# Kernel optimization log

Hardware: AMD Instinct MI355X
Metric: run time of the kernel (lower is better)

The kernel has to match this reference:

```python
import jax, jax.numpy as jnp
import numpy as np

H, HS, E, T, B, PF = 16, 64, 1024, 2048, 4, 4

def setup_inputs() -> dict:
    key = jax.random.key(0)
    ks = jax.random.split(key, 12)
    s = 0.02
    return {
        "x":  jax.random.normal(ks[0], (B, T, E), jnp.float32),
        "Wq": jax.random.normal(ks[1], (H, E, HS), jnp.float32) * s,
        "Wk": jax.random.normal(ks[2], (H, E, HS), jnp.float32) * s,
        "Wv": jax.random.normal(ks[3], (H, E, HS), jnp.float32) * s,
        "Wp": jax.random.normal(ks[4], (E, E), jnp.float32) * s,
        "bp": jnp.zeros((E,), jnp.float32),
        "W1": jax.random.normal(ks[5], (E, PF * E), jnp.float32) * s,
        "b1": jnp.zeros((PF * E,), jnp.float32),
        "W2": jax.random.normal(ks[6], (PF * E, E), jnp.float32) * s,
        "b2": jnp.zeros((E,), jnp.float32),
        "g1": jnp.ones((E,), jnp.float32),
        "be1": jnp.zeros((E,), jnp.float32),
        "g2": jnp.ones((E,), jnp.float32),
        "be2": jnp.zeros((E,), jnp.float32),
    }

def _layernorm(x, gain, bias, eps=1e-5):
    # torch.var default is unbiased (ddof=1) -- faithful to the source
    mean = jnp.mean(x, axis=-1, keepdims=True)
    var = jnp.sum((x - mean) ** 2, axis=-1, keepdims=True) / (x.shape[-1] - 1)
    return (x - mean) / jnp.sqrt(var + eps) * gain + bias

def reference(x, Wq, Wk, Wv, Wp, bp, W1, b1, W2, b2, g1, be1, g2, be2):
    Bv, Tv, Ev = x.shape
    hs = Wq.shape[-1]
    h = _layernorm(x, g1, be1)
    # all heads at once: [B,T,E] x [H,E,hs] -> [B,H,T,hs]
    q = jnp.einsum("bte,hed->bhtd", h, Wq)
    k = jnp.einsum("bte,hed->bhtd", h, Wk)
    v = jnp.einsum("bte,hed->bhtd", h, Wv)
    # NOTE: source multiplies by 1/hs**(-0.5) == sqrt(hs); kept faithful
    scores = jnp.einsum("bhtd,bhsd->bhts", q, k) * (hs ** 0.5)
    causal = jnp.tril(jnp.ones((Tv, Tv), bool))
    scores = jnp.where(causal, scores, -jnp.inf)
    w = jax.nn.softmax(scores, axis=-1)
    o = jnp.einsum("bhts,bhsd->bhtd", w, v)
    # concat heads (head 0 first) -> [B,T,H*hs]
    o = o.transpose(0, 2, 1, 3).reshape(Bv, Tv, -1)
    o = o @ Wp + bp
    x = x + o
    h2 = _layernorm(x, g2, be2)
    ff = jax.nn.relu(h2 @ W1 + b1) @ W2 + b2
    return x + ff
```

## Files before the change

### kernel.cpp

```cpp
#include <hip/hip_runtime.h>
#include <hip/hip_bf16.h>
#include <cstdint>

typedef __bf16 bf16_t;
typedef bf16_t bf16x8 __attribute__((ext_vector_type(8)));
typedef float f32x4 __attribute__((ext_vector_type(4)));

#define DEVI __device__ __forceinline__

DEVI void gload_lds16(const void* g, void* l) {
    __builtin_amdgcn_global_load_lds((const __attribute__((address_space(1))) void*)g,
                                     (__attribute__((address_space(3))) void*)l, 16, 0, 0);
}

__global__ __launch_bounds__(256) void transpose_f32_bf16(
    const float* __restrict__ src, bf16_t* __restrict__ dst,
    int ldsrc, int lddst, long srcBatchStride, long dstBatchStride)
{
    __shared__ float tile[32][33];
    src += (long)blockIdx.z * srcBatchStride;
    dst += (long)blockIdx.z * dstBatchStride;
    const int bx = blockIdx.x * 32;
    const int by = blockIdx.y * 32;
    const int tx = threadIdx.x, ty = threadIdx.y;
    #pragma unroll
    for (int j = 0; j < 32; j += 8)
        tile[ty + j][tx] = src[(size_t)(by + ty + j) * ldsrc + bx + tx];
    __syncthreads();
    #pragma unroll
    for (int j = 0; j < 32; j += 8)
        dst[(size_t)(bx + ty + j) * lddst + by + tx] = (bf16_t)tile[tx][ty + j];
}

__global__ __launch_bounds__(256) void ln_kernel(
    const float* __restrict__ x, const float* __restrict__ g,
    const float* __restrict__ b, bf16_t* __restrict__ out)
{
    const int row = blockIdx.x;
    const int tid = threadIdx.x;
    __shared__ float red[8];
    const float4 v = ((const float4*)(x + (size_t)row * 1024))[tid];
    float s = v.x + v.y + v.z + v.w;
    #pragma unroll
    for (int m = 32; m; m >>= 1) s += __shfl_xor(s, m);
    if ((tid & 63) == 0) red[tid >> 6] = s;
    __syncthreads();
    const float mean = (red[0] + red[1] + red[2] + red[3]) * (1.f / 1024.f);
    const float dx = v.x - mean, dy = v.y - mean, dz = v.z - mean, dw = v.w - mean;
    float ss = dx * dx + dy * dy + dz * dz + dw * dw;
    #pragma unroll
    for (int m = 32; m; m >>= 1) ss += __shfl_xor(ss, m);
    if ((tid & 63) == 0) red[4 + (tid >> 6)] = ss;
    __syncthreads();
    const float var = (red[4] + red[5] + red[6] + red[7]) * (1.f / 1023.f);
    const float rstd = rsqrtf(var + 1e-5f);
    const float4 gv = ((const float4*)g)[tid];
    const float4 bv = ((const float4*)b)[tid];
    union { bf16_t h[4]; uint2 u; } pk;
    pk.h[0] = (bf16_t)(dx * rstd * gv.x + bv.x);
    pk.h[1] = (bf16_t)(dy * rstd * gv.y + bv.y);
    pk.h[2] = (bf16_t)(dz * rstd * gv.z + bv.z);
    pk.h[3] = (bf16_t)(dw * rstd * gv.w + bv.w);
    *((uint2*)(out + (size_t)row * 1024 + tid * 4)) = pk.u;
}

template <int EPI>
__global__ __launch_bounds__(256) void gemm_bt(
    const bf16_t* __restrict__ A, const bf16_t* __restrict__ BT,
    void* __restrict__ Cout, const float* __restrict__ bias,
    const float* __restrict__ res, int M, int N, int K)
{
    constexpr int BK = 64;
    __shared__ bf16_t As[128 * BK];
    __shared__ bf16_t Bs[128 * BK];
    const int tid = threadIdx.x;
    const int lane = tid & 63;
    const int wid = tid >> 6;
    const int m0 = blockIdx.y * 128, n0 = blockIdx.x * 128;
    const int lrow = lane & 15, lgrp = lane >> 4;
    const int mw = (wid >> 1) * 64, nw = (wid & 1) * 64;
    f32x4 acc[4][4] = {};

    for (int k0 = 0; k0 < K; k0 += BK) {
        __syncthreads();
        #pragma unroll
        for (int i = 0; i < 4; ++i) {
            const int c = i * 256 + tid;
            const int row = c >> 3, kc = (c & 7) * 8;
            gload_lds16(A + (size_t)(m0 + row) * K + k0 + kc, &As[c * 8]);
        }
        #pragma unroll
        for (int i = 0; i < 4; ++i) {
            const int c = i * 256 + tid;
            const int row = c >> 3, kc = (c & 7) * 8;
            gload_lds16(BT + (size_t)(n0 + row) * K + k0 + kc, &Bs[c * 8]);
        }
        __syncthreads();
        #pragma unroll
        for (int kk = 0; kk < BK; kk += 32) {
            bf16x8 af[4], bfr[4];
            #pragma unroll
            for (int mi = 0; mi < 4; ++mi)
                af[mi] = *(const bf16x8*)&As[(mw + mi * 16 + lrow) * BK + kk + lgrp * 8];
            #pragma unroll
            for (int ni = 0; ni < 4; ++ni)
                bfr[ni] = *(const bf16x8*)&Bs[(nw + ni * 16 + lrow) * BK + kk + lgrp * 8];
            #pragma unroll
            for (int mi = 0; mi < 4; ++mi)
                #pragma unroll
                for (int ni = 0; ni < 4; ++ni)
                    acc[mi][ni] = __builtin_amdgcn_mfma_f32_16x16x32_bf16(
                        af[mi], bfr[ni], acc[mi][ni], 0, 0, 0);
        }
    }

    #pragma unroll
    for (int mi = 0; mi < 4; ++mi) {
        #pragma unroll
        for (int r = 0; r < 4; ++r) {
            const int row = m0 + mw + mi * 16 + lgrp * 4 + r;
            #pragma unroll
            for (int ni = 0; ni < 4; ++ni) {
                const int col = n0 + nw + ni * 16 + lrow;
                const float v = acc[mi][ni][r];
                if (EPI == 0) {
                    ((bf16_t*)Cout)[(size_t)row * N + col] = (bf16_t)v;
                } else if (EPI == 1) {
                    ((float*)Cout)[(size_t)row * N + col] =
                        v + bias[col] + res[(size_t)row * N + col];
                } else {
                    const float t = v + bias[col];
                    ((bf16_t*)Cout)[(size_t)row * N + col] = (bf16_t)(t > 0.f ? t : 0.f);
                }
            }
        }
    }
}

__global__ __launch_bounds__(256) void attn_kernel(
    const bf16_t* __restrict__ qkv, bf16_t* __restrict__ O)
{
    const int tid = threadIdx.x, lane = tid & 63, wid = tid >> 6;
    const int lrow = lane & 15, lgrp = lane >> 4;
    const int qb = (15 - blockIdx.x) * 128;
    const int b = blockIdx.y >> 4, h = blockIdx.y & 15;
    const bf16_t* base  = qkv + (size_t)b * 2048 * 3072;
    const bf16_t* Kbase = base + 1024 + h * 64;
    const bf16_t* Vbase = base + 2048 + h * 64;

    __shared__ bf16_t Vt[64 * 64];
    __shared__ bf16_t Pl[4][32 * 64];

    const int mw = wid * 32;

    bf16x8 qf[2][2];
    #pragma unroll
    for (int mi = 0; mi < 2; ++mi)
        #pragma unroll
        for (int dh = 0; dh < 2; ++dh) {
            bf16x8 t = *(const bf16x8*)(base + (size_t)(qb + mw + mi * 16 + lrow) * 3072
                                        + h * 64 + dh * 32 + lgrp * 8);
            #pragma unroll
            for (int j = 0; j < 8; ++j) t[j] = (bf16_t)((float)t[j] * 8.0f);
            qf[mi][dh] = t;
        }

    f32x4 of[2][4] = {};
    float m_r[2][4], l_r[2][4];
    #pragma unroll
    for (int mi = 0; mi < 2; ++mi)
        #pragma unroll
        for (int r = 0; r < 4; ++r) { m_r[mi][r] = -INFINITY; l_r[mi][r] = 0.f; }

    const int kvlen = qb + 128;
    for (int kv = 0; kv < kvlen; kv += 64) {
        __syncthreads();
        #pragma unroll
        for (int i = 0; i < 2; ++i) {
            const int key = tid & 63;
            const int dc8 = (tid >> 6) + i * 4;
            const bf16x8 vv = *(const bf16x8*)(Vbase + (size_t)(kv + key) * 3072 + dc8 * 8);
            #pragma unroll
            for (int j = 0; j < 8; ++j)
                Vt[(dc8 * 8 + j) * 64 + (((key >> 3) ^ j) << 3) + (key & 7)] = vv[j];
        }
        __syncthreads();

        const bool act0 = (kv <= qb + mw + 15);
        const bool act1 = (kv <= qb + mw + 31);
        if (act1) {
            bf16x8 kf[4][2];
            #pragma unroll
            for (int kt = 0; kt < 4; ++kt)
                #pragma unroll
                for (int dh = 0; dh < 2; ++dh)
                    kf[kt][dh] = *(const bf16x8*)(Kbase + (size_t)(kv + kt * 16 + lrow) * 3072
                                                  + dh * 32 + lgrp * 8);

            #pragma unroll
            for (int mi = 0; mi < 2; ++mi) {
                if (mi == 0 && !act0) continue;
                f32x4 s[4] = {};
                #pragma unroll
                for (int kt = 0; kt < 4; ++kt) {
                    s[kt] = __builtin_amdgcn_mfma_f32_16x16x32_bf16(qf[mi][0], kf[kt][0], s[kt], 0, 0, 0);
                    s[kt] = __builtin_amdgcn_mfma_f32_16x16x32_bf16(qf[mi][1], kf[kt][1], s[kt], 0, 0, 0);
                }
                float p[4][4];
                #pragma unroll
                for (int r = 0; r < 4; ++r) {
                    const int q = qb + mw + mi * 16 + lgrp * 4 + r;
                    float v0 = (kv + 0 * 16 + lrow <= q) ? s[0][r] : -INFINITY;
                    float v1 = (kv + 1 * 16 + lrow <= q) ? s[1][r] : -INFINITY;
                    float v2 = (kv + 2 * 16 + lrow <= q) ? s[2][r] : -INFINITY;
                    float v3 = (kv + 3 * 16 + lrow <= q) ? s[3][r] : -INFINITY;
                    float mx = fmaxf(fmaxf(v0, v1), fmaxf(v2, v3));
                    #pragma unroll
                    for (int mm = 8; mm; mm >>= 1) mx = fmaxf(mx, __shfl_xor(mx, mm));
                    const float mnew = fmaxf(m_r[mi][r], mx);
                    const float alpha = __expf(m_r[mi][r] - mnew);
                    p[0][r] = __expf(v0 - mnew);
                    p[1][r] = __expf(v1 - mnew);
                    p[2][r] = __expf(v2 - mnew);
                    p[3][r] = __expf(v3 - mnew);
                    float rs = p[0][r] + p[1][r] + p[2][r] + p[3][r];
                    #pragma unroll
                    for (int mm = 8; mm; mm >>= 1) rs += __shfl_xor(rs, mm);
                    l_r[mi][r] = l_r[mi][r] * alpha + rs;
                    m_r[mi][r] = mnew;
                    #pragma unroll
                    for (int dg = 0; dg < 4; ++dg) of[mi][dg][r] *= alpha;
                }
                #pragma unroll
                for (int kt = 0; kt < 4; ++kt)
                    #pragma unroll
                    for (int r = 0; r < 4; ++r) {
                        const int qi = mi * 16 + lgrp * 4 + r;
                        const int ki = kt * 16 + lrow;
                        Pl[wid][qi * 64 + ((((ki >> 3) ^ (qi & 7))) << 3) + (ki & 7)] = (bf16_t)p[kt][r];
                    }
            }
            asm volatile("s_waitcnt lgkmcnt(0)" ::: "memory");
            __builtin_amdgcn_sched_barrier(0);

            bf16x8 vf[4][2];
            #pragma unroll
            for (int dg = 0; dg < 4; ++dg) {
                const int d = dg * 16 + lrow;
                #pragma unroll
                for (int kh = 0; kh < 2; ++kh)
                    vf[dg][kh] = *(const bf16x8*)&Vt[d * 64 + ((((kh * 4 + lgrp) ^ (d & 7))) << 3)];
            }
            #pragma unroll
            for (int mi = 0; mi < 2; ++mi) {
                if (mi == 0 && !act0) continue;
                const int qrow = mi * 16 + lrow;
                #pragma unroll
                for (int kh = 0; kh < 2; ++kh) {
                    const bf16x8 pf = *(const bf16x8*)&Pl[wid][qrow * 64 + ((((kh * 4 + lgrp) ^ (lrow & 7))) << 3)];
                    #pragma unroll
                    for (int dg = 0; dg < 4; ++dg)
                        of[mi][dg] = __builtin_amdgcn_mfma_f32_16x16x32_bf16(pf, vf[dg][kh], of[mi][dg], 0, 0, 0);
                }
            }
        }
    }

    #pragma unroll
    for (int mi = 0; mi < 2; ++mi)
        #pragma unroll
        for (int dg = 0; dg < 4; ++dg)
            #pragma unroll
            for (int r = 0; r < 4; ++r) {
                const size_t row = (size_t)b * 2048 + qb + mw + mi * 16 + lgrp * 4 + r;
                O[row * 1024 + h * 64 + dg * 16 + lrow] = (bf16_t)(of[mi][dg][r] / l_r[mi][r]);
            }
}

extern "C" void kernel_launch(void* const* d_in, const int* in_sizes, int n_in,
                              void* d_out, int out_size, void* d_ws, size_t ws_size,
                              hipStream_t stream)
{
    const float* x   = (const float*)d_in[0];
    const float* Wq  = (const float*)d_in[1];
    const float* Wk  = (const float*)d_in[2];
    const float* Wv  = (const float*)d_in[3];
    const float* Wp  = (const float*)d_in[4];
    const float* bp  = (const float*)d_in[5];
    const float* W1  = (const float*)d_in[6];
    const float* b1  = (const float*)d_in[7];
    const float* W2  = (const float*)d_in[8];
    const float* b2  = (const float*)d_in[9];
    const float* g1  = (const float*)d_in[10];
    const float* be1 = (const float*)d_in[11];
    const float* g2  = (const float*)d_in[12];
    const float* be2 = (const float*)d_in[13];

    char* w = (char*)d_ws;
    auto alloc = [&](size_t bytes) { char* p = w; w += (bytes + 255) & ~255ull; return p; };
    bf16_t* wqkvT = (bf16_t*)alloc((size_t)3072 * 1024 * 2);
    bf16_t* wpT   = (bf16_t*)alloc((size_t)1024 * 1024 * 2);
    bf16_t* w1T   = (bf16_t*)alloc((size_t)4096 * 1024 * 2);
    bf16_t* w2T   = (bf16_t*)alloc((size_t)1024 * 4096 * 2);
    bf16_t* h     = (bf16_t*)alloc((size_t)8192 * 1024 * 2);
    bf16_t* qkv   = (bf16_t*)alloc((size_t)8192 * 3072 * 2);
    float*  x2    = (float*)alloc((size_t)8192 * 1024 * 4);
    bf16_t* act   = (bf16_t*)alloc((size_t)8192 * 4096 * 2);
    bf16_t* o     = h;
    bf16_t* h2    = qkv;

    const dim3 tblk(32, 8);
    transpose_f32_bf16<<<dim3(2, 32, 16), tblk, 0, stream>>>(Wq, wqkvT,                64, 1024, 1024 * 64, 64 * 1024);
    transpose_f32_bf16<<<dim3(2, 32, 16), tblk, 0, stream>>>(Wk, wqkvT + 1024 * 1024,  64, 1024, 1024 * 64, 64 * 1024);
    transpose_f32_bf16<<<dim3(2, 32, 16), tblk, 0, stream>>>(Wv, wqkvT + 2048 * 1024,  64, 1024, 1024 * 64, 64 * 1024);
    transpose_f32_bf16<<<dim3(32, 32, 1),  tblk, 0, stream>>>(Wp, wpT, 1024, 1024, 0, 0);
    transpose_f32_bf16<<<dim3(128, 32, 1), tblk, 0, stream>>>(W1, w1T, 4096, 1024, 0, 0);
    transpose_f32_bf16<<<dim3(32, 128, 1), tblk, 0, stream>>>(W2, w2T, 1024, 4096, 0, 0);

    ln_kernel<<<8192, 256, 0, stream>>>(x, g1, be1, h);
    gemm_bt<0><<<dim3(24, 64), 256, 0, stream>>>(h, wqkvT, qkv, nullptr, nullptr, 8192, 3072, 1024);
    attn_kernel<<<dim3(16, 64), 256, 0, stream>>>(qkv, o);
    gemm_bt<1><<<dim3(8, 64), 256, 0, stream>>>(o, wpT, x2, bp, x, 8192, 1024, 1024);
    ln_kernel<<<8192, 256, 0, stream>>>(x2, g2, be2, h2);
    gemm_bt<2><<<dim3(32, 64), 256, 0, stream>>>(h2, w1T, act, b1, nullptr, 8192, 4096, 1024);
    gemm_bt<1><<<dim3(8, 64), 256, 0, stream>>>(act, w2T, d_out, b2, x2, 8192, 1024, 4096);
}
```

Before: 769.4 us.

## Pair causal query blocks per CTA and prefetch next K/V tile into registers

Each attention block now handles two query tiles (jq and 15-jq), so every CTA does the same amount of causal work and the grid shrinks to 8x64. K and V for the next 64-key tile are loaded into registers while the current tile is computed, hiding global load latency. The row-sum shuffle reduction moves out of the inner loop to a single reduction at the end, and s_setprio wraps the MFMA sections. The cost is higher register pressure from the prefetch buffers and fewer, longer blocks, which may lower occupancy.

```diff
diff --git a/kernel.cpp b/kernel.cpp
--- a/kernel.cpp
+++ b/kernel.cpp
@@ -142,7 +142,6 @@
 {
     const int tid = threadIdx.x, lane = tid & 63, wid = tid >> 6;
     const int lrow = lane & 15, lgrp = lane >> 4;
-    const int qb = (15 - blockIdx.x) * 128;
     const int b = blockIdx.y >> 4, h = blockIdx.y & 15;
     const bf16_t* base  = qkv + (size_t)b * 2048 * 3072;
     const bf16_t* Kbase = base + 1024 + h * 64;
@@ -152,129 +151,172 @@
     __shared__ bf16_t Pl[4][32 * 64];
 
     const int mw = wid * 32;
-
-    bf16x8 qf[2][2];
-    #pragma unroll
-    for (int mi = 0; mi < 2; ++mi)
-        #pragma unroll
-        for (int dh = 0; dh < 2; ++dh) {
-            bf16x8 t = *(const bf16x8*)(base + (size_t)(qb + mw + mi * 16 + lrow) * 3072
-                                        + h * 64 + dh * 32 + lgrp * 8);
-            #pragma unroll
-            for (int j = 0; j < 8; ++j) t[j] = (bf16_t)((float)t[j] * 8.0f);
-            qf[mi][dh] = t;
-        }
-
-    f32x4 of[2][4] = {};
-    float m_r[2][4], l_r[2][4];
-    #pragma unroll
-    for (int mi = 0; mi < 2; ++mi)
-        #pragma unroll
-        for (int r = 0; r < 4; ++r) { m_r[mi][r] = -INFINITY; l_r[mi][r] = 0.f; }
-
-    const int kvlen = qb + 128;
-    for (int kv = 0; kv < kvlen; kv += 64) {
-        __syncthreads();
-        #pragma unroll
-        for (int i = 0; i < 2; ++i) {
-            const int key = tid & 63;
-            const int dc8 = (tid >> 6) + i * 4;
-            const bf16x8 vv = *(const bf16x8*)(Vbase + (size_t)(kv + key) * 3072 + dc8 * 8);
-            #pragma unroll
-            for (int j = 0; j < 8; ++j)
-                Vt[(dc8 * 8 + j) * 64 + (((key >> 3) ^ j) << 3) + (key & 7)] = vv[j];
-        }
-        __syncthreads();
-
-        const bool act0 = (kv <= qb + mw + 15);
-        const bool act1 = (kv <= qb + mw + 31);
-        if (act1) {
-            bf16x8 kf[4][2];
-            #pragma unroll
-            for (int kt = 0; kt < 4; ++kt)
-                #pragma unroll
-                for (int dh = 0; dh < 2; ++dh)
-                    kf[kt][dh] = *(const bf16x8*)(Kbase + (size_t)(kv + kt * 16 + lrow) * 3072
-                                                  + dh * 32 + lgrp * 8);
-
-            #pragma unroll
-            for (int mi = 0; mi < 2; ++mi) {
-                if (mi == 0 && !act0) continue;
-                f32x4 s[4] = {};
-                #pragma unroll
-                for (int kt = 0; kt < 4; ++kt) {
-                    s[kt] = __builtin_amdgcn_mfma_f32_16x16x32_bf16(qf[mi][0], kf[kt][0], s[kt], 0, 0, 0);
-                    s[kt] = __builtin_amdgcn_mfma_f32_16x16x32_bf16(qf[mi][1], kf[kt][1], s[kt], 0, 0, 0);
-                }
-                float p[4][4];
+    const int vkey = tid & 63;
+    const int vdc  = tid >> 6;
+
+    for (int pass = 0; pass < 2; ++pass) {
+        const int jq = (pass == 0) ? 15 - (int)blockIdx.x : (int)blockIdx.x;
+        const int qb = jq * 128;
+        const int nt = (qb + 128) >> 6;
+
+        bf16x8 qf[2][2];
+        #pragma unroll
+        for (int mi = 0; mi < 2; ++mi)
+            #pragma unroll
+            for (int dh = 0; dh < 2; ++dh) {
+                bf16x8 t = *(const bf16x8*)(base + (size_t)(qb + mw + mi * 16 + lrow) * 3072
+                                            + h * 64 + dh * 32 + lgrp * 8);
+                #pragma unroll
+                for (int j = 0; j < 8; ++j) t[j] = (bf16_t)((float)t[j] * 8.0f);
+                qf[mi][dh] = t;
+            }
+
+        f32x4 of[2][4] = {};
+        float m_r[2][4], l_r[2][4];
+        #pragma unroll
+        for (int mi = 0; mi < 2; ++mi)
+            #pragma unroll
+            for (int r = 0; r < 4; ++r) { m_r[mi][r] = -INFINITY; l_r[mi][r] = 0.f; }
+
+        bf16x8 vvc[2], kfc[4][2];
+        #pragma unroll
+        for (int i = 0; i < 2; ++i)
+            vvc[i] = *(const bf16x8*)(Vbase + (size_t)vkey * 3072 + (vdc + i * 4) * 8);
+        #pragma unroll
+        for (int kt = 0; kt < 4; ++kt)
+            #pragma unroll
+            for (int dh = 0; dh < 2; ++dh)
+                kfc[kt][dh] = *(const bf16x8*)(Kbase + (size_t)(kt * 16 + lrow) * 3072
+                                               + dh * 32 + lgrp * 8);
+
+        for (int t = 0; t < nt; ++t) {
+            const int kv = t << 6;
+            __syncthreads();
+            #pragma unroll
+            for (int i = 0; i < 2; ++i) {
+                const int dc8 = vdc + i * 4;
+                #pragma unroll
+                for (int j = 0; j < 8; ++j)
+                    Vt[(dc8 * 8 + j) * 64 + (((vkey >> 3) ^ j) << 3) + (vkey & 7)] = vvc[i][j];
+            }
+            __syncthreads();
+
+            bf16x8 vvn[2], kfn[4][2];
+            const bool hasn = (t + 1 < nt);
+            if (hasn) {
+                const int kv2 = kv + 64;
+                #pragma unroll
+                for (int i = 0; i < 2; ++i)
+                    vvn[i] = *(const bf16x8*)(Vbase + (size_t)(kv2 + vkey) * 3072 + (vdc + i * 4) * 8);
+                #pragma unroll
+                for (int kt = 0; kt < 4; ++kt)
+                    #pragma unroll
+                    for (int dh = 0; dh < 2; ++dh)
+                        kfn[kt][dh] = *(const bf16x8*)(Kbase + (size_t)(kv2 + kt * 16 + lrow) * 3072
+                                                       + dh * 32 + lgrp * 8);
+            }
+
+            const bool act0 = (kv <= qb + mw + 15);
+            const bool act1 = (kv <= qb + mw + 31);
+            if (act1) {
+                #pragma unroll
+                for (int mi = 0; mi < 2; ++mi) {
+                    if (mi == 0 && !act0) continue;
+                    f32x4 s[4] = {};
+                    __builtin_amdgcn_s_setprio(1);
+                    #pragma unroll
+                    for (int kt = 0; kt < 4; ++kt) {
+                        s[kt] = __builtin_amdgcn_mfma_f32_16x16x32_bf16(qf[mi][0], kfc[kt][0], s[kt], 0, 0, 0);
+                        s[kt] = __builtin_amdgcn_mfma_f32_16x16x32_bf16(qf[mi][1], kfc[kt][1], s[kt], 0, 0, 0);
+                    }
+                    __builtin_amdgcn_s_setprio(0);
+                    float p[4][4];
+                    #pragma unroll
+                    for (int r = 0; r < 4; ++r) {
+                        const int q = qb + mw + mi * 16 + lgrp * 4 + r;
+                        float v0 = (kv + 0 * 16 + lrow <= q) ? s[0][r] : -INFINITY;
+                        float v1 = (kv + 1 * 16 + lrow <= q) ? s[1][r] : -INFINITY;
+                        float v2 = (kv + 2 * 16 + lrow <= q) ? s[2][r] : -INFINITY;
+                        float v3 = (kv + 3 * 16 + lrow <= q) ? s[3][r] : -INFINITY;
+                        float mx = fmaxf(fmaxf(v0, v1), fmaxf(v2, v3));
+                        #pragma unroll
+                        for (int mm = 8; mm; mm >>= 1) mx = fmaxf(mx, __shfl_xor(mx, mm));
+                        const float mnew = fmaxf(m_r[mi][r], mx);
+                        const float alpha = __expf(m_r[mi][r] - mnew);
+                        p[0][r] = __expf(v0 - mnew);
+                        p[1][r] = __expf(v1 - mnew);
+                        p[2][r] = __expf(v2 - mnew);
+                        p[3][r] = __expf(v3 - mnew);
+                        l_r[mi][r] = l_r[mi][r] * alpha + (p[0][r] + p[1][r] + p[2][r] + p[3][r]);
+                        m_r[mi][r] = mnew;
+                        #pragma unroll
+                        for (int dg = 0; dg < 4; ++dg) of[mi][dg][r] *= alpha;
+                    }
+                    #pragma unroll
+                    for (int kt = 0; kt < 4; ++kt)
+                        #pragma unroll
+                        for (int r = 0; r < 4; ++r) {
+                            const int qi = mi * 16 + lgrp * 4 + r;
+                            const int ki = kt * 16 + lrow;
+                            Pl[wid][qi * 64 + ((((ki >> 3) ^ (qi & 7))) << 3) + (ki & 7)] = (bf16_t)p[kt][r];
+                        }
+                }
+                asm volatile("s_waitcnt lgkmcnt(0)" ::: "memory");
+                __builtin_amdgcn_sched_barrier(0);
+
+                bf16x8 vf[4][2];
+                #pragma unroll
+                for (int dg = 0; dg < 4; ++dg) {
+                    const int d = dg * 16 + lrow;
+                    #pragma unroll
+                    for (int kh = 0; kh < 2; ++kh)
+                        vf[dg][kh] = *(const bf16x8*)&Vt[d * 64 + ((((kh * 4 + lgrp) ^ (d & 7))) << 3)];
+                }
+                __builtin_amdgcn_s_setprio(1);
+                #pragma unroll
+                for (int mi = 0; mi < 2; ++mi) {
+                    if (mi == 0 && !act0) continue;
+                    const int qrow = mi * 16 + lrow;
+                    #pragma unroll
+                    for (int kh = 0; kh < 2; ++kh) {
+                        const bf16x8 pf = *(const bf16x8*)&Pl[wid][qrow * 64 + ((((kh * 4 + lgrp) ^ (lrow & 7))) << 3)];
+                        #pragma unroll
+                        for (int dg = 0; dg < 4; ++dg)
+                            of[mi][dg] = __builtin_amdgcn_mfma_f32_16x16x32_bf16(pf, vf[dg][kh], of[mi][dg], 0, 0, 0);
+                    }
+                }
+                __builtin_amdgcn_s_setprio(0);
+            }
+
+            if (hasn) {
+                #pragma unroll
+                for (int i = 0; i < 2; ++i) vvc[i] = vvn[i];
+                #pragma unroll
+                for (int kt = 0; kt < 4; ++kt)
+                    #pragma unroll
+                    for (int dh = 0; dh < 2; ++dh) kfc[kt][dh] = kfn[kt][dh];
+            }
+        }
+
+        #pragma unroll
+        for (int mi = 0; mi < 2; ++mi)
+            #pragma unroll
+            for (int r = 0; r < 4; ++r) {
+                float l = l_r[mi][r];
+                #pragma unroll
+                for (int mm = 8; mm; mm >>= 1) l += __shfl_xor(l, mm);
+                l_r[mi][r] = l;
+            }
+        #pragma unroll
+        for (int mi = 0; mi < 2; ++mi)
+            #pragma unroll
+            for (int dg = 0; dg < 4; ++dg)
                 #pragma unroll
                 for (int r = 0; r < 4; ++r) {
-                    const int q = qb + mw + mi * 16 + lgrp * 4 + r;
-                    float v0 = (kv + 0 * 16 + lrow <= q) ? s[0][r] : -INFINITY;
-                    float v1 = (kv + 1 * 16 + lrow <= q) ? s[1][r] : -INFINITY;
-                    float v2 = (kv + 2 * 16 + lrow <= q) ? s[2][r] : -INFINITY;
-                    float v3 = (kv + 3 * 16 + lrow <= q) ? s[3][r] : -INFINITY;
-                    float mx = fmaxf(fmaxf(v0, v1), fmaxf(v2, v3));
-                    #pragma unroll
-                    for (int mm = 8; mm; mm >>= 1) mx = fmaxf(mx, __shfl_xor(mx, mm));
-                    const float mnew = fmaxf(m_r[mi][r], mx);
-                    const float alpha = __expf(m_r[mi][r] - mnew);
-                    p[0][r] = __expf(v0 - mnew);
-                    p[1][r] = __expf(v1 - mnew);
-                    p[2][r] = __expf(v2 - mnew);
-                    p[3][r] = __expf(v3 - mnew);
-                    float rs = p[0][r] + p[1][r] + p[2][r] + p[3][r];
-                    #pragma unroll
-                    for (int mm = 8; mm; mm >>= 1) rs += __shfl_xor(rs, mm);
-                    l_r[mi][r] = l_r[mi][r] * alpha + rs;
-                    m_r[mi][r] = mnew;
-                    #pragma unroll
-                    for (int dg = 0; dg < 4; ++dg) of[mi][dg][r] *= alpha;
-                }
-                #pragma unroll
-                for (int kt = 0; kt < 4; ++kt)
-                    #pragma unroll
-                    for (int r = 0; r < 4; ++r) {
-                        const int qi = mi * 16 + lgrp * 4 + r;
-                        const int ki = kt * 16 + lrow;
-                        Pl[wid][qi * 64 + ((((ki >> 3) ^ (qi & 7))) << 3) + (ki & 7)] = (bf16_t)p[kt][r];
-                    }
-            }
-            asm volatile("s_waitcnt lgkmcnt(0)" ::: "memory");
-            __builtin_amdgcn_sched_barrier(0);
-
-            bf16x8 vf[4][2];
-            #pragma unroll
-            for (int dg = 0; dg < 4; ++dg) {
-                const int d = dg * 16 + lrow;
-                #pragma unroll
-                for (int kh = 0; kh < 2; ++kh)
-                    vf[dg][kh] = *(const bf16x8*)&Vt[d * 64 + ((((kh * 4 + lgrp) ^ (d & 7))) << 3)];
-            }
-            #pragma unroll
-            for (int mi = 0; mi < 2; ++mi) {
-                if (mi == 0 && !act0) continue;
-                const int qrow = mi * 16 + lrow;
-                #pragma unroll
-                for (int kh = 0; kh < 2; ++kh) {
-                    const bf16x8 pf = *(const bf16x8*)&Pl[wid][qrow * 64 + ((((kh * 4 + lgrp) ^ (lrow & 7))) << 3)];
-                    #pragma unroll
-                    for (int dg = 0; dg < 4; ++dg)
-                        of[mi][dg] = __builtin_amdgcn_mfma_f32_16x16x32_bf16(pf, vf[dg][kh], of[mi][dg], 0, 0, 0);
-                }
-            }
-        }
+                    const size_t row = (size_t)b * 2048 + qb + mw + mi * 16 + lgrp * 4 + r;
+                    O[row * 1024 + h * 64 + dg * 16 + lrow] = (bf16_t)(of[mi][dg][r] / l_r[mi][r]);
+                }
     }
-
-    #pragma unroll
-    for (int mi = 0; mi < 2; ++mi)
-        #pragma unroll
-        for (int dg = 0; dg < 4; ++dg)
-            #pragma unroll
-            for (int r = 0; r < 4; ++r) {
-                const size_t row = (size_t)b * 2048 + qb + mw + mi * 16 + lgrp * 4 + r;
-                O[row * 1024 + h * 64 + dg * 16 + lrow] = (bf16_t)(of[mi][dg][r] / l_r[mi][r]);
-            }
 }
 
 extern "C" void kernel_launch(void* const* d_in, const int* in_sizes, int n_in,
@@ -319,7 +361,7 @@
 
     ln_kernel<<<8192, 256, 0, stream>>>(x, g1, be1, h);
     gemm_bt<0><<<dim3(24, 64), 256, 0, stream>>>(h, wqkvT, qkv, nullptr, nullptr, 8192, 3072, 1024);
-    attn_kernel<<<dim3(16, 64), 256, 0, stream>>>(qkv, o);
+    attn_kernel<<<dim3(8, 64), 256, 0, stream>>>(qkv, o);
     gemm_bt<1><<<dim3(8, 64), 256, 0, stream>>>(o, wpT, x2, bp, x, 8192, 1024, 1024);
     ln_kernel<<<8192, 256, 0, stream>>>(x2, g2, be2, h2);
     gemm_bt<2><<<dim3(32, 64), 256, 0, stream>>>(h2, w1T, act, b1, nullptr, 8192, 4096, 1024);
```

Measured after the change: 698.7 us. 9.2% less time.

## Rewrite attention as persistent kernel with atomic work queue and register-resident P

Applied to the files above, without the earlier changes.

The attention kernel becomes persistent: 768 blocks pull (query-tile, batch-head) tasks from an atomic counter, longest causal tiles first, with 64-row query tiles and 16 rows per wave. It computes S transposed so the probabilities can be handed to the PV MFMA via lane shuffles instead of an LDS round trip. It also double-buffers V in LDS, prefetches the next K/V tile into registers, and applies the causal mask only on the diagonal tile. A lazy rescale skips the softmax correction unless the max grows by more than 8. The aim is better load balance across the triangular workload and less LDS traffic and synchronisation, at the cost of an extra memset, an atomic per task and more register pressure.

```diff
diff --git a/kernel.cpp b/kernel.cpp
--- a/kernel.cpp
+++ b/kernel.cpp
@@ -137,144 +137,183 @@
     }
 }
 
-__global__ __launch_bounds__(256) void attn_kernel(
-    const bf16_t* __restrict__ qkv, bf16_t* __restrict__ O)
+__global__ __launch_bounds__(256, 3) void attn_kernel(
+    const bf16_t* __restrict__ qkv, bf16_t* __restrict__ O, int* __restrict__ ctr)
 {
     const int tid = threadIdx.x, lane = tid & 63, wid = tid >> 6;
     const int lrow = lane & 15, lgrp = lane >> 4;
-    const int qb = (15 - blockIdx.x) * 128;
-    const int b = blockIdx.y >> 4, h = blockIdx.y & 15;
-    const bf16_t* base  = qkv + (size_t)b * 2048 * 3072;
-    const bf16_t* Kbase = base + 1024 + h * 64;
-    const bf16_t* Vbase = base + 2048 + h * 64;
-
-    __shared__ bf16_t Vt[64 * 64];
-    __shared__ bf16_t Pl[4][32 * 64];
-
-    const int mw = wid * 32;
-
-    bf16x8 qf[2][2];
-    #pragma unroll
-    for (int mi = 0; mi < 2; ++mi)
+
+    __shared__ bf16_t Vt[2][64 * 64];
+    __shared__ int s_task;
+
+    const int srcA = lrow + ((lgrp & 1) << 5);
+    const int srcB = srcA + 16;
+    const bool selHi = ((lgrp >> 1) & 1) != 0;
+
+    const int vp  = (tid & 31) * 2;
+    const int vdc = tid >> 5;
+
+    for (;;) {
+        __syncthreads();
+        if (tid == 0) s_task = atomicAdd(ctr, 1);
+        __syncthreads();
+        const int task = s_task;
+        if (task >= 2048) return;
+
+        const int qt = 31 - (task >> 6);
+        const int bh = task & 63;
+        const int b = bh >> 4, h = bh & 15;
+        const bf16_t* base  = qkv + (size_t)b * 2048 * 3072;
+        const bf16_t* Kbase = base + 1024 + h * 64;
+        const bf16_t* Vbase = base + 2048 + h * 64;
+        const int qb = qt * 64;
+        const int nt = qt + 1;
+        const int qrow = qb + wid * 16 + lrow;
+
+        bf16x8 qf[2];
         #pragma unroll
         for (int dh = 0; dh < 2; ++dh) {
-            bf16x8 t = *(const bf16x8*)(base + (size_t)(qb + mw + mi * 16 + lrow) * 3072
-                                        + h * 64 + dh * 32 + lgrp * 8);
+            bf16x8 t = *(const bf16x8*)(base + (size_t)qrow * 3072 + h * 64 + dh * 32 + lgrp * 8);
             #pragma unroll
             for (int j = 0; j < 8; ++j) t[j] = (bf16_t)((float)t[j] * 8.0f);
-            qf[mi][dh] = t;
-        }
-
-    f32x4 of[2][4] = {};
-    float m_r[2][4], l_r[2][4];
-    #pragma unroll
-    for (int mi = 0; mi < 2; ++mi)
-        #pragma unroll
-        for (int r = 0; r < 4; ++r) { m_r[mi][r] = -INFINITY; l_r[mi][r] = 0.f; }
-
-    const int kvlen = qb + 128;
-    for (int kv = 0; kv < kvlen; kv += 64) {
-        __syncthreads();
-        #pragma unroll
-        for (int i = 0; i < 2; ++i) {
-            const int key = tid & 63;
-            const int dc8 = (tid >> 6) + i * 4;
-            const bf16x8 vv = *(const bf16x8*)(Vbase + (size_t)(kv + key) * 3072 + dc8 * 8);
-            #pragma unroll
-            for (int j = 0; j < 8; ++j)
-                Vt[(dc8 * 8 + j) * 64 + (((key >> 3) ^ j) << 3) + (key & 7)] = vv[j];
-        }
-        __syncthreads();
-
-        const bool act0 = (kv <= qb + mw + 15);
-        const bool act1 = (kv <= qb + mw + 31);
-        if (act1) {
-            bf16x8 kf[4][2];
-            #pragma unroll
-            for (int kt = 0; kt < 4; ++kt)
-                #pragma unroll
-                for (int dh = 0; dh < 2; ++dh)
-                    kf[kt][dh] = *(const bf16x8*)(Kbase + (size_t)(kv + kt * 16 + lrow) * 3072
-                                                  + dh * 32 + lgrp * 8);
-
-            #pragma unroll
-            for (int mi = 0; mi < 2; ++mi) {
-                if (mi == 0 && !act0) continue;
-                f32x4 s[4] = {};
-                #pragma unroll
-                for (int kt = 0; kt < 4; ++kt) {
-                    s[kt] = __builtin_amdgcn_mfma_f32_16x16x32_bf16(qf[mi][0], kf[kt][0], s[kt], 0, 0, 0);
-                    s[kt] = __builtin_amdgcn_mfma_f32_16x16x32_bf16(qf[mi][1], kf[kt][1], s[kt], 0, 0, 0);
-                }
-                float p[4][4];
-                #pragma unroll
-                for (int r = 0; r < 4; ++r) {
-                    const int q = qb + mw + mi * 16 + lgrp * 4 + r;
-                    float v0 = (kv + 0 * 16 + lrow <= q) ? s[0][r] : -INFINITY;
-                    float v1 = (kv + 1 * 16 + lrow <= q) ? s[1][r] : -INFINITY;
-                    float v2 = (kv + 2 * 16 + lrow <= q) ? s[2][r] : -INFINITY;
-                    float v3 = (kv + 3 * 16 + lrow <= q) ? s[3][r] : -INFINITY;
-                    float mx = fmaxf(fmaxf(v0, v1), fmaxf(v2, v3));
-                    #pragma unroll
-                    for (int mm = 8; mm; mm >>= 1) mx = fmaxf(mx, __shfl_xor(mx, mm));
-                    const float mnew = fmaxf(m_r[mi][r], mx);
-                    const float alpha = __expf(m_r[mi][r] - mnew);
-                    p[0][r] = __expf(v0 - mnew);
-                    p[1][r] = __expf(v1 - mnew);
-                    p[2][r] = __expf(v2 - mnew);
-                    p[3][r] = __expf(v3 - mnew);
-                    float rs = p[0][r] + p[1][r] + p[2][r] + p[3][r];
-                    #pragma unroll
-                    for (int mm = 8; mm; mm >>= 1) rs += __shfl_xor(rs, mm);
-                    l_r[mi][r] = l_r[mi][r] * alpha + rs;
-                    m_r[mi][r] = mnew;
-                    #pragma unroll
-                    for (int dg = 0; dg < 4; ++dg) of[mi][dg][r] *= alpha;
-                }
+            qf[dh] = t;
+        }
+
+        f32x4 of[4] = {};
+        float m = -1e30f, lp = 0.f;
+
+        bf16x8 vvc0 = *(const bf16x8*)(Vbase + (size_t)(vp    ) * 3072 + vdc * 8);
+        bf16x8 vvc1 = *(const bf16x8*)(Vbase + (size_t)(vp + 1) * 3072 + vdc * 8);
+        bf16x8 kf[4][2];
+        #pragma unroll
+        for (int kt = 0; kt < 4; ++kt)
+            #pragma unroll
+            for (int dh = 0; dh < 2; ++dh)
+                kf[kt][dh] = *(const bf16x8*)(Kbase + (size_t)(kt * 16 + lrow) * 3072 + dh * 32 + lgrp * 8);
+
+        int cb = 0;
+        for (int t = 0; t < nt; ++t) {
+            bf16_t* vt = Vt[cb];
+            #pragma unroll
+            for (int j = 0; j < 8; ++j) {
+                const int d = vdc * 8 + j;
+                union { bf16_t h2[2]; uint32_t u; } w2;
+                w2.h2[0] = vvc0[j]; w2.h2[1] = vvc1[j];
+                *(uint32_t*)&vt[d * 64 + (((vp >> 3) ^ (d & 7)) << 3) + (vp & 7)] = w2.u;
+            }
+
+            const bool hasn = (t + 1 < nt);
+            bf16x8 vvn0, vvn1, kfn[4][2];
+            if (hasn) {
+                const int kv2 = (t + 1) << 6;
+                vvn0 = *(const bf16x8*)(Vbase + (size_t)(kv2 + vp    ) * 3072 + vdc * 8);
+                vvn1 = *(const bf16x8*)(Vbase + (size_t)(kv2 + vp + 1) * 3072 + vdc * 8);
                 #pragma unroll
                 for (int kt = 0; kt < 4; ++kt)
                     #pragma unroll
-                    for (int r = 0; r < 4; ++r) {
-                        const int qi = mi * 16 + lgrp * 4 + r;
-                        const int ki = kt * 16 + lrow;
-                        Pl[wid][qi * 64 + ((((ki >> 3) ^ (qi & 7))) << 3) + (ki & 7)] = (bf16_t)p[kt][r];
-                    }
-            }
-            asm volatile("s_waitcnt lgkmcnt(0)" ::: "memory");
-            __builtin_amdgcn_sched_barrier(0);
-
-            bf16x8 vf[4][2];
-            #pragma unroll
-            for (int dg = 0; dg < 4; ++dg) {
-                const int d = dg * 16 + lrow;
-                #pragma unroll
-                for (int kh = 0; kh < 2; ++kh)
-                    vf[dg][kh] = *(const bf16x8*)&Vt[d * 64 + ((((kh * 4 + lgrp) ^ (d & 7))) << 3)];
-            }
-            #pragma unroll
-            for (int mi = 0; mi < 2; ++mi) {
-                if (mi == 0 && !act0) continue;
-                const int qrow = mi * 16 + lrow;
-                #pragma unroll
-                for (int kh = 0; kh < 2; ++kh) {
-                    const bf16x8 pf = *(const bf16x8*)&Pl[wid][qrow * 64 + ((((kh * 4 + lgrp) ^ (lrow & 7))) << 3)];
+                    for (int dh = 0; dh < 2; ++dh)
+                        kfn[kt][dh] = *(const bf16x8*)(Kbase + (size_t)(kv2 + kt * 16 + lrow) * 3072
+                                                       + dh * 32 + lgrp * 8);
+            }
+
+            f32x4 sT[4] = {};
+            __builtin_amdgcn_s_setprio(1);
+            #pragma unroll
+            for (int kt = 0; kt < 4; ++kt) {
+                sT[kt] = __builtin_amdgcn_mfma_f32_16x16x32_bf16(kf[kt][0], qf[0], sT[kt], 0, 0, 0);
+                sT[kt] = __builtin_amdgcn_mfma_f32_16x16x32_bf16(kf[kt][1], qf[1], sT[kt], 0, 0, 0);
+            }
+            __builtin_amdgcn_s_setprio(0);
+
+            if (t == nt - 1) {
+                #pragma unroll
+                for (int kt = 0; kt < 4; ++kt)
                     #pragma unroll
-                    for (int dg = 0; dg < 4; ++dg)
-                        of[mi][dg] = __builtin_amdgcn_mfma_f32_16x16x32_bf16(pf, vf[dg][kh], of[mi][dg], 0, 0, 0);
+                    for (int r = 0; r < 4; ++r)
+                        if (kt * 16 + lgrp * 4 + r > wid * 16 + lrow) sT[kt][r] = -INFINITY;
+            }
+
+            float pmax = -INFINITY;
+            #pragma unroll
+            for (int kt = 0; kt < 4; ++kt)
+                pmax = fmaxf(pmax, fmaxf(fmaxf(sT[kt][0], sT[kt][1]), fmaxf(sT[kt][2], sT[kt][3])));
+            pmax = fmaxf(pmax, __shfl_xor(pmax, 16));
+            pmax = fmaxf(pmax, __shfl_xor(pmax, 32));
+            if (__any(pmax > m + 8.f)) {
+                const float mnew = fmaxf(m, pmax);
+                const float alpha = __expf(m - mnew);
+                m = mnew;
+                lp *= alpha;
+                #pragma unroll
+                for (int dg = 0; dg < 4; ++dg) of[dg] *= alpha;
+            }
+            uint32_t pk[4][2];
+            float sum = 0.f;
+            #pragma unroll
+            for (int kt = 0; kt < 4; ++kt) {
+                const float p0 = __expf(sT[kt][0] - m), p1 = __expf(sT[kt][1] - m);
+                const float p2 = __expf(sT[kt][2] - m), p3 = __expf(sT[kt][3] - m);
+                sum += (p0 + p1) + (p2 + p3);
+                union { bf16_t h2[2]; uint32_t u; } w0, w1;
+                w0.h2[0] = (bf16_t)p0; w0.h2[1] = (bf16_t)p1;
+                w1.h2[0] = (bf16_t)p2; w1.h2[1] = (bf16_t)p3;
+                pk[kt][0] = w0.u; pk[kt][1] = w1.u;
+            }
+            lp += sum;
+
+            uint32_t W[2][4];
+            #pragma unroll
+            for (int kh = 0; kh < 2; ++kh) {
+                const int k0 = kh * 2, k1 = kh * 2 + 1;
+                const uint32_t a0 = __shfl(pk[k0][0], srcA), b0 = __shfl(pk[k1][0], srcA);
+                const uint32_t a1 = __shfl(pk[k0][1], srcA), b1 = __shfl(pk[k1][1], srcA);
+                const uint32_t a2 = __shfl(pk[k0][0], srcB), b2 = __shfl(pk[k1][0], srcB);
+                const uint32_t a3 = __shfl(pk[k0][1], srcB), b3 = __shfl(pk[k1][1], srcB);
+                W[kh][0] = selHi ? b0 : a0;
+                W[kh][1] = selHi ? b1 : a1;
+                W[kh][2] = selHi ? b2 : a2;
+                W[kh][3] = selHi ? b3 : a3;
+            }
+
+            asm volatile("s_waitcnt lgkmcnt(0)\n\ts_barrier" ::: "memory");
+
+            __builtin_amdgcn_s_setprio(1);
+            #pragma unroll
+            for (int kh = 0; kh < 2; ++kh) {
+                union { uint32_t u[4]; bf16x8 v; } pb;
+                pb.u[0] = W[kh][0]; pb.u[1] = W[kh][1]; pb.u[2] = W[kh][2]; pb.u[3] = W[kh][3];
+                #pragma unroll
+                for (int dg = 0; dg < 4; ++dg) {
+                    const int d = dg * 16 + lrow;
+                    const bf16x8 vf = *(const bf16x8*)&vt[d * 64 + (((kh * 4 + lgrp) ^ (d & 7)) << 3)];
+                    of[dg] = __builtin_amdgcn_mfma_f32_16x16x32_bf16(vf, pb.v, of[dg], 0, 0, 0);
                 }
             }
+            __builtin_amdgcn_s_setprio(0);
+
+            if (hasn) {
+                vvc0 = vvn0; vvc1 = vvn1;
+                #pragma unroll
+                for (int kt = 0; kt < 4; ++kt) {
+                    kf[kt][0] = kfn[kt][0];
+                    kf[kt][1] = kfn[kt][1];
+                }
+            }
+            cb ^= 1;
+        }
+
+        lp += __shfl_xor(lp, 16);
+        lp += __shfl_xor(lp, 32);
+        const float rl = 1.f / lp;
+        bf16_t* orow = O + (size_t)(b * 2048 + qrow) * 1024 + h * 64;
+        #pragma unroll
+        for (int dg = 0; dg < 4; ++dg) {
+            union { bf16_t h4[4]; uint2 u; } w;
+            #pragma unroll
+            for (int r = 0; r < 4; ++r) w.h4[r] = (bf16_t)(of[dg][r] * rl);
+            *(uint2*)&orow[dg * 16 + lgrp * 4] = w.u;
         }
     }
-
-    #pragma unroll
-    for (int mi = 0; mi < 2; ++mi)
-        #pragma unroll
-        for (int dg = 0; dg < 4; ++dg)
-            #pragma unroll
-            for (int r = 0; r < 4; ++r) {
-                const size_t row = (size_t)b * 2048 + qb + mw + mi * 16 + lgrp * 4 + r;
-                O[row * 1024 + h * 64 + dg * 16 + lrow] = (bf16_t)(of[mi][dg][r] / l_r[mi][r]);
-            }
 }
 
 extern "C" void kernel_launch(void* const* d_in, const int* in_sizes, int n_in,
@@ -306,8 +345,11 @@
     bf16_t* qkv   = (bf16_t*)alloc((size_t)8192 * 3072 * 2);
     float*  x2    = (float*)alloc((size_t)8192 * 1024 * 4);
     bf16_t* act   = (bf16_t*)alloc((size_t)8192 * 4096 * 2);
+    int*    ctr   = (int*)alloc(256);
     bf16_t* o     = h;
     bf16_t* h2    = qkv;
+
+    hipMemsetAsync(ctr, 0, 4, stream);
 
     const dim3 tblk(32, 8);
     transpose_f32_bf16<<<dim3(2, 32, 16), tblk, 0, stream>>>(Wq, wqkvT,                64, 1024, 1024 * 64, 64 * 1024);
@@ -319,7 +361,7 @@
 
     ln_kernel<<<8192, 256, 0, stream>>>(x, g1, be1, h);
     gemm_bt<0><<<dim3(24, 64), 256, 0, stream>>>(h, wqkvT, qkv, nullptr, nullptr, 8192, 3072, 1024);
-    attn_kernel<<<dim3(16, 64), 256, 0, stream>>>(qkv, o);
+    attn_kernel<<<768, 256, 0, stream>>>(qkv, o, ctr);
     gemm_bt<1><<<dim3(8, 64), 256, 0, stream>>>(o, wpT, x2, bp, x, 8192, 1024, 1024);
     ln_kernel<<<8192, 256, 0, stream>>>(x2, g2, be2, h2);
     gemm_bt<2><<<dim3(32, 64), 256, 0, stream>>>(h2, w1T, act, b1, nullptr, 8192, 4096, 1024);
```

After: 645.3 us. 16.1% less time.
